# Kernel optimization log

Hardware: AMD Instinct MI355X
Metric: run time of the kernel (lower is better)

Reference implementation:

```python
import jax, jax.numpy as jnp
import numpy as np

H = 8          # n_heads
MRF = 128      # max_rf random features
EPS = 1e-4


def fiber2head(feats, h):
    # feats: list of [N, m_d, 2d+1] -> [N, h, sum_d (m_d/h)*(2d+1)]
    N = feats[0].shape[0]
    return jnp.concatenate([f.reshape(N, h, -1) for f in feats], axis=-1)


def softmax_kernel(data, w, is_query):
    # FAVOR+ positive random features. data: [B,H,L,d], w: [m,d]
    dn = data.shape[-1] ** -0.25
    ratio = w.shape[0] ** -0.5
    dd = jnp.einsum('bhld,md->bhlm', data * dn, w)
    diag = (data * data).sum(-1, keepdims=True) * (0.5 * dn * dn)
    if is_query:
        mx = jax.lax.stop_gradient(dd.max(-1, keepdims=True))
    else:
        mx = jax.lax.stop_gradient(dd.max())
    return ratio * (jnp.exp(dd - diag - mx) + EPS)


def setup_inputs() -> dict:
    key = jax.random.key(0)
    ks = jax.random.split(key, 7)
    B, L = 4, 8192
    N = B * L
    v0 = jax.random.normal(ks[0], (N, 64, 1), jnp.float32)
    v1 = jax.random.normal(ks[1], (N, 64, 3), jnp.float32)
    k0 = jax.random.normal(ks[2], (N, 64, 1), jnp.float32)
    k1 = jax.random.normal(ks[3], (N, 64, 3), jnp.float32)
    q0 = jax.random.normal(ks[4], (N, 64, 1), jnp.float32)
    q1 = jax.random.normal(ks[5], (N, 64, 3), jnp.float32)
    w = jax.random.normal(ks[6], (MRF, 32), jnp.float32)  # random-feature projection
    return {'v0': v0, 'v1': v1, 'k0': k0, 'k1': k1, 'q0': q0, 'q1': q1, 'w': w, 'batch_size': 4}


def reference(v0, v1, k0, k1, q0, q1, w, batch_size):
    B = batch_size
    N = v0.shape[0]
    L = N // B
    # Q from the k-dict (as in source); source then overwrites K with Q, so the
    # q-dict features are mathematically unused.
    Q = fiber2head([k0, k1], H).reshape(B, L, H, -1).transpose(0, 2, 1, 3)  # [B,H,L,d_k]
    K = Q  # faithful to `K = Q.view(...)` in the source
    Kp = softmax_kernel(K, w, is_query=False)  # [B,H,L,m]
    Qp = softmax_kernel(Q, w, is_query=True)   # [B,H,L,m]
    # Normalizer is identical for every value channel (q/k are expanded copies).
    D_inv = 1.0 / jnp.einsum('bhlm,bhm->bhl', Qp, Kp.sum(axis=2))
    outs = []
    for v in (v0, v1):
        m, e = v.shape[1], v.shape[2]     # multiplicity, 2d+1
        c = m // H                         # channels per head
        vv = v.reshape(B, L, H, c, e).transpose(0, 2, 3, 1, 4)  # [B,H,c,L,e]
        # linear attention: context [B,H,c,m,e] is small -> O(L*m*e) traffic
        ctx = jnp.einsum('bhlm,bhcle->bhcme', Kp, vv)
        o = jnp.einsum('bhcme,bhlm,bhl->bhcle', ctx, Qp, D_inv)
        o = o.reshape(B, H * c, L, e).transpose(0, 2, 1, 3).reshape(B * L, c * H, e)
        outs.append(o)
    return tuple(outs)  # (out_deg0 [N,64,1], out_deg1 [N,64,3])
```

## Files before the change

### kernel.cpp

```cpp
#include <hip/hip_runtime.h>

#define BB 4
#define HH 8
#define LL 8192
#define NN (BB*LL)
#define DDIM 32
#define MM 128

#define CTXR_OFF 0
#define KSUMR_OFF (CTXR_OFF + 32*8*MM*4)
#define VSUM_OFF  (KSUMR_OFF + 32*MM)
#define GMAX_OFF  (VSUM_OFF + 32*32)
#define ZERO_FLOATS (GMAX_OFF + 1)

#define DN 0.42044820762685725f
#define RATIO 0.08838834764831845f
#define EPSF 1e-4f

#define ACC_UPDATE(kp, a0, a1, b4)                                     \
    do {                                                               \
        acc[0]  = fmaf(kp,(a0).x,acc[0]);   acc[4]  = fmaf(kp,(a0).y,acc[4]);  \
        acc[8]  = fmaf(kp,(a0).z,acc[8]);   acc[12] = fmaf(kp,(a0).w,acc[12]); \
        acc[16] = fmaf(kp,(a1).x,acc[16]);  acc[20] = fmaf(kp,(a1).y,acc[20]); \
        acc[24] = fmaf(kp,(a1).z,acc[24]);  acc[28] = fmaf(kp,(a1).w,acc[28]); \
        float4 g;                                                      \
        g = (b4)[0];                                                   \
        acc[1]=fmaf(kp,g.x,acc[1]);  acc[2]=fmaf(kp,g.y,acc[2]);       \
        acc[3]=fmaf(kp,g.z,acc[3]);  acc[5]=fmaf(kp,g.w,acc[5]);       \
        g = (b4)[1];                                                   \
        acc[6]=fmaf(kp,g.x,acc[6]);  acc[7]=fmaf(kp,g.y,acc[7]);       \
        acc[9]=fmaf(kp,g.z,acc[9]);  acc[10]=fmaf(kp,g.w,acc[10]);     \
        g = (b4)[2];                                                   \
        acc[11]=fmaf(kp,g.x,acc[11]); acc[13]=fmaf(kp,g.y,acc[13]);    \
        acc[14]=fmaf(kp,g.z,acc[14]); acc[15]=fmaf(kp,g.w,acc[15]);    \
        g = (b4)[3];                                                   \
        acc[17]=fmaf(kp,g.x,acc[17]); acc[18]=fmaf(kp,g.y,acc[18]);    \
        acc[19]=fmaf(kp,g.z,acc[19]); acc[21]=fmaf(kp,g.w,acc[21]);    \
        g = (b4)[4];                                                   \
        acc[22]=fmaf(kp,g.x,acc[22]); acc[23]=fmaf(kp,g.y,acc[23]);    \
        acc[25]=fmaf(kp,g.z,acc[25]); acc[26]=fmaf(kp,g.w,acc[26]);    \
        g = (b4)[5];                                                   \
        acc[27]=fmaf(kp,g.x,acc[27]); acc[29]=fmaf(kp,g.y,acc[29]);    \
        acc[30]=fmaf(kp,g.z,acc[30]); acc[31]=fmaf(kp,g.w,acc[31]);    \
    } while (0)

__global__ __launch_bounds__(256, 2) void k_ctx1(const float* __restrict__ kk0,
                                                 const float* __restrict__ kk1,
                                                 const float* __restrict__ v0,
                                                 const float* __restrict__ v1,
                                                 const float* __restrict__ w,
                                                 float* __restrict__ ws) {
    __shared__ float red[2][64][34];
    const int tid = threadIdx.x;
    const int lane = tid & 63;
    const int wv  = __builtin_amdgcn_readfirstlane(tid >> 6);
    const int bh = blockIdx.x >> 6;
    const int chunk = (blockIdx.x >> 1) & 31;
    const int mhalf = blockIdx.x & 1;
    const int m = mhalf*64 + lane;
    const int b = bh >> 3, h = bh & 7;
    const int n0 = b*LL + chunk*256 + wv*64;
    float wreg[32];
    {
        const float4* w4 = (const float4*)(w + m*DDIM);
#pragma unroll
        for (int q = 0; q < 8; ++q) {
            const float4 t = w4[q];
            wreg[q*4+0]=t.x*DN; wreg[q*4+1]=t.y*DN;
            wreg[q*4+2]=t.z*DN; wreg[q*4+3]=t.w*DN;
        }
    }
    float acc[32];
#pragma unroll
    for (int i = 0; i < 32; ++i) acc[i] = 0.f;
    float ksum_acc = 0.f, vsum_acc = 0.f, wmax = -3.4e38f;
    for (int s = 0; s < 4; ++s) {
        const int nb = n0 + s*16;
        const int dr_ = lane >> 2, dq = lane & 3;
        float diagv;
        {
            const int n = nb + dr_;
            float4 da, db;
            if (dq == 0) {
                da = *(const float4*)(kk0 + (size_t)n*64 + h*8);
                db = *(const float4*)(kk0 + (size_t)n*64 + h*8 + 4);
            } else {
                const float* bp = kk1 + (size_t)n*192 + h*24 + (dq-1)*8;
                da = *(const float4*)bp; db = *(const float4*)(bp + 4);
            }
            float ss = da.x*da.x+da.y*da.y+da.z*da.z+da.w*da.w
                     + db.x*db.x+db.y*db.y+db.z*db.z+db.w*db.w;
            ss += __shfl_xor(ss, 1); ss += __shfl_xor(ss, 2);
            diagv = 0.5f*DN*DN*ss;
        }
        if (mhalf == 0) {
            const int ve = lane & 31, vg = lane >> 5;
#pragma unroll
            for (int rr = 0; rr < 8; ++rr) {
                const int n = nb + vg*8 + rr;
                vsum_acc += (ve < 8) ? v0[(size_t)n*64 + h*8 + ve]
                                     : v1[(size_t)n*192 + h*24 + (ve-8)];
            }
        }
#pragma unroll 1
        for (int r = 0; r < 16; r += 2) {
            const int nA = nb + r, nB = nb + r + 1;
            const float dgA = __uint_as_float(
                __builtin_amdgcn_readlane(__float_as_uint(diagv), r*4));
            const float dgB = __uint_as_float(
                __builtin_amdgcn_readlane(__float_as_uint(diagv), r*4 + 4));
            float4 kA[8], kB[8];
            kA[0] = *(const float4*)(kk0 + (size_t)nA*64 + h*8);
            kA[1] = *(const float4*)(kk0 + (size_t)nA*64 + h*8 + 4);
            kB[0] = *(const float4*)(kk0 + (size_t)nB*64 + h*8);
            kB[1] = *(const float4*)(kk0 + (size_t)nB*64 + h*8 + 4);
            {
                const float4* gA4 = (const float4*)(kk1 + (size_t)nA*192 + h*24);
                const float4* gB4 = (const float4*)(kk1 + (size_t)nB*192 + h*24);
#pragma unroll
                for (int gq = 0; gq < 6; ++gq) { kA[2+gq] = gA4[gq]; kB[2+gq] = gB4[gq]; }
            }
            float ddA0 = 0.f, ddA1 = 0.f, ddB0 = 0.f, ddB1 = 0.f;
#pragma unroll
            for (int q = 0; q < 8; ++q) {
                ddA0 = fmaf(kA[q].x, wreg[q*4+0], ddA0);
                ddB0 = fmaf(kB[q].x, wreg[q*4+0], ddB0);
                ddA1 = fmaf(kA[q].y, wreg[q*4+1], ddA1);
                ddB1 = fmaf(kB[q].y, wreg[q*4+1], ddB1);
                ddA0 = fmaf(kA[q].z, wreg[q*4+2], ddA0);
                ddB0 = fmaf(kB[q].z, wreg[q*4+2], ddB0);
                ddA1 = fmaf(kA[q].w, wreg[q*4+3], ddA1);
                ddB1 = fmaf(kB[q].w, wreg[q*4+3], ddB1);
            }
            const float ddA = ddA0 + ddA1;
            const float ddB = ddB0 + ddB1;
            wmax = fmaxf(wmax, fmaxf(ddA, ddB));
            const float kpA = __expf(ddA - dgA);
            const float kpB = __expf(ddB - dgB);
            ksum_acc += kpA; ksum_acc += kpB;
            const float4 aA0 = *(const float4*)(v0 + (size_t)nA*64 + h*8);
            const float4 aA1 = *(const float4*)(v0 + (size_t)nA*64 + h*8 + 4);
            const float4 aB0 = *(const float4*)(v0 + (size_t)nB*64 + h*8);
            const float4 aB1 = *(const float4*)(v0 + (size_t)nB*64 + h*8 + 4);
            const float4* bA4 = (const float4*)(v1 + (size_t)nA*192 + h*24);
            const float4* bB4 = (const float4*)(v1 + (size_t)nB*192 + h*24);
            ACC_UPDATE(kpA, aA0, aA1, bA4);
            ACC_UPDATE(kpB, aB0, aB1, bB4);
        }
    }
    if (wv == 1 || wv == 3) {
        float (*rp)[34] = red[wv >> 1];
#pragma unroll
        for (int i = 0; i < 32; ++i) rp[lane][i] = acc[i];
        rp[lane][32] = ksum_acc;
        rp[lane][33] = vsum_acc;
    }
    __syncthreads();
    if (wv == 0 || wv == 2) {
        float (*rp)[34] = red[wv >> 1];
#pragma unroll
        for (int i = 0; i < 32; ++i) acc[i] += rp[lane][i];
        ksum_acc += rp[lane][32];
        vsum_acc += rp[lane][33];
    }
    __syncthreads();
    if (wv == 2) {
#pragma unroll
        for (int i = 0; i < 32; ++i) red[0][lane][i] = acc[i];
        red[0][lane][32] = ksum_acc;
        red[0][lane][33] = vsum_acc;
    }
    __syncthreads();
    if (wv == 0) {
#pragma unroll
        for (int i = 0; i < 32; ++i) acc[i] += red[0][lane][i];
        ksum_acc += red[0][lane][32];
        vsum_acc += red[0][lane][33];
        float* ctxr = ws + CTXR_OFF;
#pragma unroll
        for (int c = 0; c < 8; ++c)
#pragma unroll
            for (int j = 0; j < 4; ++j)
                atomicAdd(&ctxr[((bh*8 + c)*MM + m)*4 + j], acc[c*4+j]);
        atomicAdd(ws + KSUMR_OFF + bh*MM + m, ksum_acc);
        if (mhalf == 0) {
            const int ve = lane & 31;
            const int packed = (ve < 8) ? ve*4
                                        : ((ve-8)/3)*4 + 1 + (ve-8)%3;
            atomicAdd(ws + VSUM_OFF + bh*32 + packed, vsum_acc);
        }
    }
#pragma unroll
    for (int off = 32; off; off >>= 1) wmax = fmaxf(wmax, __shfl_xor(wmax, off, 64));
    if (lane == 0) {
        unsigned u = __float_as_uint(wmax);
        u = (u & 0x80000000u) ? ~u : (u | 0x80000000u);
        atomicMax((unsigned*)(ws + GMAX_OFF), u);
    }
}

__global__ __launch_bounds__(256, 1) void k_out(const float* __restrict__ kk0,
                                                const float* __restrict__ kk1,
                                                const float* __restrict__ w,
                                                const float* __restrict__ ws,
                                                float* __restrict__ out) {
    __shared__ float ctx_s[128*36];
    __shared__ float wlds[128*36];
    __shared__ float ksl[128];
    __shared__ __align__(16) float sS0[32];
    __shared__ float sK0;
    const int tid = threadIdx.x;
    const int bh = blockIdx.x >> 4, chunk = blockIdx.x & 15;
    const int b = bh >> 3, h = bh & 7;
    const unsigned gu = *((const unsigned*)(ws + GMAX_OFF));
    const float gm = (gu & 0x80000000u) ? __uint_as_float(gu & 0x7fffffffu)
                                        : __uint_as_float(~gu);
    const float alpha = __expf(-gm);
    const float4* ctxr4 = (const float4*)(ws + CTXR_OFF) + (size_t)bh*1024;
    const float* vsg = ws + VSUM_OFF + bh*32;
#pragma unroll
    for (int it = 0; it < 4; ++it) {
        const int i = tid + it*256;
        const int c = i >> 7, mm2 = i & 127;
        const float4 q = ctxr4[i];
        const int p0 = c*4;
        ctx_s[mm2*36+p0+0] = RATIO*(alpha*q.x + EPSF*vsg[p0+0]);
        ctx_s[mm2*36+p0+1] = RATIO*(alpha*q.y + EPSF*vsg[p0+1]);
        ctx_s[mm2*36+p0+2] = RATIO*(alpha*q.z + EPSF*vsg[p0+2]);
        ctx_s[mm2*36+p0+3] = RATIO*(alpha*q.w + EPSF*vsg[p0+3]);
    }
    {
        const float4* w4 = (const float4*)w;
#pragma unroll
        for (int it = 0; it < 4; ++it) {
            const int i = tid + it*256;
            const int mm2 = i >> 3, q = i & 7;
            float4 t = w4[i];
            t.x*=DN; t.y*=DN; t.z*=DN; t.w*=DN;
            *(float4*)&wlds[mm2*36+q*4] = t;
        }
    }
    if (tid < 128) ksl[tid] = RATIO*(alpha*ws[KSUMR_OFF + bh*MM + tid] + EPSF*(float)LL);
    __syncthreads();
    if (tid < 32) {
        float s = 0.f;
#pragma unroll 8
        for (int mm2 = 0; mm2 < 128; ++mm2) s += ctx_s[mm2*36 + tid];
        sS0[tid] = s;
    } else if (tid < 64) {
        const int p2 = tid - 32;
        float s = ksl[p2] + ksl[32+p2] + ksl[64+p2] + ksl[96+p2];
        s += __shfl_xor(s, 1); s += __shfl_xor(s, 2); s += __shfl_xor(s, 4);
        s += __shfl_xor(s, 8); s += __shfl_xor(s, 16);
        if (p2 == 0) sK0 = s;
    }
    __syncthreads();
    const int nA = b*LL + chunk*512 + tid;
    const int nB = nA + 256;
    float KA[32], KB[32];
    {
        const float4 f0 = *(const float4*)(kk0 + (size_t)nA*64 + h*8);
        const float4 f1 = *(const float4*)(kk0 + (size_t)nA*64 + h*8 + 4);
        KA[0]=f0.x; KA[1]=f0.y; KA[2]=f0.z; KA[3]=f0.w;
        KA[4]=f1.x; KA[5]=f1.y; KA[6]=f1.z; KA[7]=f1.w;
        const float4 g0 = *(const float4*)(kk0 + (size_t)nB*64 + h*8);
        const float4 g1 = *(const float4*)(kk0 + (size_t)nB*64 + h*8 + 4);
        KB[0]=g0.x; KB[1]=g0.y; KB[2]=g0.z; KB[3]=g0.w;
        KB[4]=g1.x; KB[5]=g1.y; KB[6]=g1.z; KB[7]=g1.w;
        const float4* a4 = (const float4*)(kk1 + (size_t)nA*192 + h*24);
        const float4* b4 = (const float4*)(kk1 + (size_t)nB*192 + h*24);
#pragma unroll
        for (int gq = 0; gq < 6; ++gq) {
            const float4 ga = a4[gq];
            KA[8+gq*4+0]=ga.x; KA[8+gq*4+1]=ga.y; KA[8+gq*4+2]=ga.z; KA[8+gq*4+3]=ga.w;
            const float4 gb = b4[gq];
            KB[8+gq*4+0]=gb.x; KB[8+gq*4+1]=gb.y; KB[8+gq*4+2]=gb.z; KB[8+gq*4+3]=gb.w;
        }
    }
    float dgA = 0.f, dgB = 0.f;
#pragma unroll
    for (int d = 0; d < 32; ++d) { dgA = fmaf(KA[d], KA[d], dgA); dgB = fmaf(KB[d], KB[d], dgB); }
    dgA *= 0.5f*DN*DN;  dgB *= 0.5f*DN*DN;
    float S1A[32], S1B[32];
#pragma unroll
    for (int i = 0; i < 32; ++i) { S1A[i] = 0.f; S1B[i] = 0.f; }
    float denA = 0.f, denB = 0.f, mxA = -3.4e38f, mxB = -3.4e38f;
#pragma unroll 1
    for (int m2 = 0; m2 < 128; ++m2) {
        const float* wrow = &wlds[m2*36];
        float dA0 = 0.f, dA1 = 0.f, dB0 = 0.f, dB1 = 0.f;
#pragma unroll
        for (int q = 0; q < 8; ++q) {
            const float4 wv = *(const float4*)&wrow[q*4];
            dA0 = fmaf(KA[q*4+0], wv.x, dA0);
            dB0 = fmaf(KB[q*4+0], wv.x, dB0);
            dA1 = fmaf(KA[q*4+1], wv.y, dA1);
            dB1 = fmaf(KB[q*4+1], wv.y, dB1);
            dA0 = fmaf(KA[q*4+2], wv.z, dA0);
            dB0 = fmaf(KB[q*4+2], wv.z, dB0);
            dA1 = fmaf(KA[q*4+3], wv.w, dA1);
            dB1 = fmaf(KB[q*4+3], wv.w, dB1);
        }
        const float ddA = dA0 + dA1;
        const float ddB = dB0 + dB1;
        mxA = fmaxf(mxA, ddA);
        mxB = fmaxf(mxB, ddB);
        const float EA = __expf(ddA - dgA);
        const float EB = __expf(ddB - dgB);
        denA = fmaf(EA, ksl[m2], denA);
        denB = fmaf(EB, ksl[m2], denB);
        const float* crow = &ctx_s[m2*36];
#pragma unroll
        for (int q = 0; q < 8; ++q) {
            const float4 cv = *(const float4*)&crow[q*4];
            S1A[q*4+0] = fmaf(EA, cv.x, S1A[q*4+0]);
            S1B[q*4+0] = fmaf(EB, cv.x, S1B[q*4+0]);
            S1A[q*4+1] = fmaf(EA, cv.y, S1A[q*4+1]);
            S1B[q*4+1] = fmaf(EB, cv.y, S1B[q*4+1]);
            S1A[q*4+2] = fmaf(EA, cv.z, S1A[q*4+2]);
            S1B[q*4+2] = fmaf(EB, cv.z, S1B[q*4+2]);
            S1A[q*4+3] = fmaf(EA, cv.w, S1A[q*4+3]);
            S1B[q*4+3] = fmaf(EB, cv.w, S1B[q*4+3]);
        }
    }
    const float esA = __expf(-mxA);
    const float esB = __expf(-mxB);
    const float dinvA = 1.f / fmaf(esA, denA, EPSF*sK0);
    const float dinvB = 1.f / fmaf(esB, denB, EPSF*sK0);
    float vA[32], vB[32];
#pragma unroll
    for (int q = 0; q < 8; ++q) {
        const float4 s0 = *(const float4*)&sS0[q*4];
        vA[q*4+0] = fmaf(esA, S1A[q*4+0], EPSF*s0.x)*dinvA;
        vA[q*4+1] = fmaf(esA, S1A[q*4+1], EPSF*s0.y)*dinvA;
        vA[q*4+2] = fmaf(esA, S1A[q*4+2], EPSF*s0.z)*dinvA;
        vA[q*4+3] = fmaf(esA, S1A[q*4+3], EPSF*s0.w)*dinvA;
        vB[q*4+0] = fmaf(esB, S1B[q*4+0], EPSF*s0.x)*dinvB;
        vB[q*4+1] = fmaf(esB, S1B[q*4+1], EPSF*s0.y)*dinvB;
        vB[q*4+2] = fmaf(esB, S1B[q*4+2], EPSF*s0.z)*dinvB;
        vB[q*4+3] = fmaf(esB, S1B[q*4+3], EPSF*s0.w)*dinvB;
    }
    {
        float* o0 = out + (size_t)nA*64 + h*8;
        *(float4*)(o0)     = make_float4(vA[0],  vA[4],  vA[8],  vA[12]);
        *(float4*)(o0 + 4) = make_float4(vA[16], vA[20], vA[24], vA[28]);
        float* o1 = out + (size_t)NN*64 + (size_t)nA*192 + h*24;
        *(float4*)(o1 +  0) = make_float4(vA[1],  vA[2],  vA[3],  vA[5]);
        *(float4*)(o1 +  4) = make_float4(vA[6],  vA[7],  vA[9],  vA[10]);
        *(float4*)(o1 +  8) = make_float4(vA[11], vA[13], vA[14], vA[15]);
        *(float4*)(o1 + 12) = make_float4(vA[17], vA[18], vA[19], vA[21]);
        *(float4*)(o1 + 16) = make_float4(vA[22], vA[23], vA[25], vA[26]);
        *(float4*)(o1 + 20) = make_float4(vA[27], vA[29], vA[30], vA[31]);
    }
    {
        float* o0 = out + (size_t)nB*64 + h*8;
        *(float4*)(o0)     = make_float4(vB[0],  vB[4],  vB[8],  vB[12]);
        *(float4*)(o0 + 4) = make_float4(vB[16], vB[20], vB[24], vB[28]);
        float* o1 = out + (size_t)NN*64 + (size_t)nB*192 + h*24;
        *(float4*)(o1 +  0) = make_float4(vB[1],  vB[2],  vB[3],  vB[5]);
        *(float4*)(o1 +  4) = make_float4(vB[6],  vB[7],  vB[9],  vB[10]);
        *(float4*)(o1 +  8) = make_float4(vB[11], vB[13], vB[14], vB[15]);
        *(float4*)(o1 + 12) = make_float4(vB[17], vB[18], vB[19], vB[21]);
        *(float4*)(o1 + 16) = make_float4(vB[22], vB[23], vB[25], vB[26]);
        *(float4*)(o1 + 20) = make_float4(vB[27], vB[29], vB[30], vB[31]);
    }
}

extern "C" void kernel_launch(void* const* d_in, const int* in_sizes, int n_in,
                              void* d_out, int out_size, void* d_ws, size_t ws_size,
                              hipStream_t stream) {
    const float* v0 = (const float*)d_in[0];
    const float* v1 = (const float*)d_in[1];
    const float* k0 = (const float*)d_in[2];
    const float* k1 = (const float*)d_in[3];
    const float* w  = (const float*)d_in[6];
    float* out = (float*)d_out;
    float* ws  = (float*)d_ws;
    hipMemsetAsync(ws, 0, (size_t)ZERO_FLOATS*sizeof(float), stream);
    k_ctx1<<<2048, 256, 0, stream>>>(k0, k1, v0, v1, w, ws);
    k_out <<<512, 256, 0, stream>>>(k0, k1, w, ws, out);
}
```

Before: 259.9 us.

## Load K/V tiles cooperatively across lanes and broadcast via readlane

In the context-accumulation kernel, each lane no longer issues redundant wave-uniform loads of the same K and V rows. Lanes now cooperatively load a 32-row tile into registers with distributed float4 loads, and every scalar is broadcast with v_readlane in fully unrolled loops. This removes duplicated global/L1 load traffic and address arithmetic per row. In exchange it adds many readlane (SALU/VALU) instructions and larger unrolled code, with more register pressure.

Result: faster. 243.8 us (-6.2%).

```diff
diff --git a/kernel.cpp b/kernel.cpp
--- a/kernel.cpp
+++ b/kernel.cpp
@@ -17,32 +17,13 @@
 #define RATIO 0.08838834764831845f
 #define EPSF 1e-4f
 
-#define ACC_UPDATE(kp, a0, a1, b4)                                     \
-    do {                                                               \
-        acc[0]  = fmaf(kp,(a0).x,acc[0]);   acc[4]  = fmaf(kp,(a0).y,acc[4]);  \
-        acc[8]  = fmaf(kp,(a0).z,acc[8]);   acc[12] = fmaf(kp,(a0).w,acc[12]); \
-        acc[16] = fmaf(kp,(a1).x,acc[16]);  acc[20] = fmaf(kp,(a1).y,acc[20]); \
-        acc[24] = fmaf(kp,(a1).z,acc[24]);  acc[28] = fmaf(kp,(a1).w,acc[28]); \
-        float4 g;                                                      \
-        g = (b4)[0];                                                   \
-        acc[1]=fmaf(kp,g.x,acc[1]);  acc[2]=fmaf(kp,g.y,acc[2]);       \
-        acc[3]=fmaf(kp,g.z,acc[3]);  acc[5]=fmaf(kp,g.w,acc[5]);       \
-        g = (b4)[1];                                                   \
-        acc[6]=fmaf(kp,g.x,acc[6]);  acc[7]=fmaf(kp,g.y,acc[7]);       \
-        acc[9]=fmaf(kp,g.z,acc[9]);  acc[10]=fmaf(kp,g.w,acc[10]);     \
-        g = (b4)[2];                                                   \
-        acc[11]=fmaf(kp,g.x,acc[11]); acc[13]=fmaf(kp,g.y,acc[13]);    \
-        acc[14]=fmaf(kp,g.z,acc[14]); acc[15]=fmaf(kp,g.w,acc[15]);    \
-        g = (b4)[3];                                                   \
-        acc[17]=fmaf(kp,g.x,acc[17]); acc[18]=fmaf(kp,g.y,acc[18]);    \
-        acc[19]=fmaf(kp,g.z,acc[19]); acc[21]=fmaf(kp,g.w,acc[21]);    \
-        g = (b4)[4];                                                   \
-        acc[22]=fmaf(kp,g.x,acc[22]); acc[23]=fmaf(kp,g.y,acc[23]);    \
-        acc[25]=fmaf(kp,g.z,acc[25]); acc[26]=fmaf(kp,g.w,acc[26]);    \
-        g = (b4)[5];                                                   \
-        acc[27]=fmaf(kp,g.x,acc[27]); acc[29]=fmaf(kp,g.y,acc[29]);    \
-        acc[30]=fmaf(kp,g.z,acc[30]); acc[31]=fmaf(kp,g.w,acc[31]);    \
-    } while (0)
+__device__ __forceinline__ float rl(float x, int l) {
+    return __uint_as_float(__builtin_amdgcn_readlane(__float_as_uint(x), l));
+}
+__device__ __forceinline__ float rl4(float4 v, int c, int l) {
+    const float x = (c==0) ? v.x : (c==1) ? v.y : (c==2) ? v.z : v.w;
+    return rl(x, l);
+}
 
 __global__ __launch_bounds__(256, 2) void k_ctx1(const float* __restrict__ kk0,
                                                  const float* __restrict__ kk1,
@@ -70,16 +51,30 @@
             wreg[q*4+2]=t.z*DN; wreg[q*4+3]=t.w*DN;
         }
     }
+    const int rowA = lane >> 1, qA = lane & 1;
+    const int offA = rowA*64 + h*8 + qA*4;
+    const int rowB = lane >> 3, qB = lane & 7;
+    const int offB = rowB*192 + h*24 + ((qB < 6) ? qB*4 : 20);
     float acc[32];
 #pragma unroll
     for (int i = 0; i < 32; ++i) acc[i] = 0.f;
     float ksum_acc = 0.f, vsum_acc = 0.f, wmax = -3.4e38f;
-    for (int s = 0; s < 4; ++s) {
-        const int nb = n0 + s*16;
-        const int dr_ = lane >> 2, dq = lane & 3;
-        float diagv;
-        {
-            const int n = nb + dr_;
+#pragma unroll 1
+    for (int bi = 0; bi < 2; ++bi) {
+        const int nb = n0 + bi*32;
+        const float4 k0b = *(const float4*)(kk0 + (size_t)nb*64 + offA);
+        const float4 v0b = *(const float4*)(v0  + (size_t)nb*64 + offA);
+        float4 k1b[4], v1b[4];
+#pragma unroll
+        for (int j = 0; j < 4; ++j) {
+            k1b[j] = *(const float4*)(kk1 + (size_t)nb*192 + j*1536 + offB);
+            v1b[j] = *(const float4*)(v1  + (size_t)nb*192 + j*1536 + offB);
+        }
+        float diagv0, diagv1;
+#pragma unroll
+        for (int dp = 0; dp < 2; ++dp) {
+            const int dr_ = lane >> 2, dq = lane & 3;
+            const int n = nb + dp*16 + dr_;
             float4 da, db;
             if (dq == 0) {
                 da = *(const float4*)(kk0 + (size_t)n*64 + h*8);
@@ -91,61 +86,55 @@
             float ss = da.x*da.x+da.y*da.y+da.z*da.z+da.w*da.w
                      + db.x*db.x+db.y*db.y+db.z*db.z+db.w*db.w;
             ss += __shfl_xor(ss, 1); ss += __shfl_xor(ss, 2);
-            diagv = 0.5f*DN*DN*ss;
+            const float dv_ = 0.5f*DN*DN*ss;
+            if (dp == 0) diagv0 = dv_; else diagv1 = dv_;
         }
         if (mhalf == 0) {
             const int ve = lane & 31, vg = lane >> 5;
 #pragma unroll
+            for (int dp = 0; dp < 2; ++dp)
+#pragma unroll
+                for (int rr = 0; rr < 8; ++rr) {
+                    const int n = nb + dp*16 + vg*8 + rr;
+                    vsum_acc += (ve < 8) ? v0[(size_t)n*64 + h*8 + ve]
+                                         : v1[(size_t)n*192 + h*24 + (ve-8)];
+                }
+        }
+#pragma unroll
+        for (int rq = 0; rq < 4; ++rq) {
+#pragma unroll
             for (int rr = 0; rr < 8; ++rr) {
-                const int n = nb + vg*8 + rr;
-                vsum_acc += (ve < 8) ? v0[(size_t)n*64 + h*8 + ve]
-                                     : v1[(size_t)n*192 + h*24 + (ve-8)];
+                const int r = rq*8 + rr;
+                const float dg = rl((r < 16) ? diagv0 : diagv1, (r & 15)*4);
+                float dd0 = 0.f, dd1 = 0.f;
+#pragma unroll
+                for (int d = 0; d < 8; ++d) {
+                    const float s = rl4(k0b, d & 3, r*2 + (d >> 2));
+                    if (d & 1) dd1 = fmaf(s, wreg[d], dd1);
+                    else       dd0 = fmaf(s, wreg[d], dd0);
+                }
+#pragma unroll
+                for (int e = 0; e < 24; ++e) {
+                    const float s = rl4(k1b[rq], e & 3, rr*8 + (e >> 2));
+                    if (e & 1) dd1 = fmaf(s, wreg[8+e], dd1);
+                    else       dd0 = fmaf(s, wreg[8+e], dd0);
+                }
+                const float dd = dd0 + dd1;
+                wmax = fmaxf(wmax, dd);
+                const float kp = __expf(dd - dg);
+                ksum_acc += kp;
+#pragma unroll
+                for (int c = 0; c < 8; ++c) {
+                    const float av = rl4(v0b, c & 3, r*2 + (c >> 2));
+                    acc[c*4] = fmaf(kp, av, acc[c*4]);
+                }
+#pragma unroll
+                for (int e = 0; e < 24; ++e) {
+                    const float av = rl4(v1b[rq], e & 3, rr*8 + (e >> 2));
+                    const int ai = (e/3)*4 + 1 + e%3;
+                    acc[ai] = fmaf(kp, av, acc[ai]);
+                }
             }
-        }
-#pragma unroll 1
-        for (int r = 0; r < 16; r += 2) {
-            const int nA = nb + r, nB = nb + r + 1;
-            const float dgA = __uint_as_float(
-                __builtin_amdgcn_readlane(__float_as_uint(diagv), r*4));
-            const float dgB = __uint_as_float(
-                __builtin_amdgcn_readlane(__float_as_uint(diagv), r*4 + 4));
-            float4 kA[8], kB[8];
-            kA[0] = *(const float4*)(kk0 + (size_t)nA*64 + h*8);
-            kA[1] = *(const float4*)(kk0 + (size_t)nA*64 + h*8 + 4);
-            kB[0] = *(const float4*)(kk0 + (size_t)nB*64 + h*8);
-            kB[1] = *(const float4*)(kk0 + (size_t)nB*64 + h*8 + 4);
-            {
-                const float4* gA4 = (const float4*)(kk1 + (size_t)nA*192 + h*24);
-                const float4* gB4 = (const float4*)(kk1 + (size_t)nB*192 + h*24);
-#pragma unroll
-                for (int gq = 0; gq < 6; ++gq) { kA[2+gq] = gA4[gq]; kB[2+gq] = gB4[gq]; }
-            }
-            float ddA0 = 0.f, ddA1 = 0.f, ddB0 = 0.f, ddB1 = 0.f;
-#pragma unroll
-            for (int q = 0; q < 8; ++q) {
-                ddA0 = fmaf(kA[q].x, wreg[q*4+0], ddA0);
-                ddB0 = fmaf(kB[q].x, wreg[q*4+0], ddB0);
-                ddA1 = fmaf(kA[q].y, wreg[q*4+1], ddA1);
-                ddB1 = fmaf(kB[q].y, wreg[q*4+1], ddB1);
-                ddA0 = fmaf(kA[q].z, wreg[q*4+2], ddA0);
-                ddB0 = fmaf(kB[q].z, wreg[q*4+2], ddB0);
-                ddA1 = fmaf(kA[q].w, wreg[q*4+3], ddA1);
-                ddB1 = fmaf(kB[q].w, wreg[q*4+3], ddB1);
-            }
-            const float ddA = ddA0 + ddA1;
-            const float ddB = ddB0 + ddB1;
-            wmax = fmaxf(wmax, fmaxf(ddA, ddB));
-            const float kpA = __expf(ddA - dgA);
-            const float kpB = __expf(ddB - dgB);
-            ksum_acc += kpA; ksum_acc += kpB;
-            const float4 aA0 = *(const float4*)(v0 + (size_t)nA*64 + h*8);
-            const float4 aA1 = *(const float4*)(v0 + (size_t)nA*64 + h*8 + 4);
-            const float4 aB0 = *(const float4*)(v0 + (size_t)nB*64 + h*8);
-            const float4 aB1 = *(const float4*)(v0 + (size_t)nB*64 + h*8 + 4);
-            const float4* bA4 = (const float4*)(v1 + (size_t)nA*192 + h*24);
-            const float4* bB4 = (const float4*)(v1 + (size_t)nB*192 + h*24);
-            ACC_UPDATE(kpA, aA0, aA1, bA4);
-            ACC_UPDATE(kpB, aB0, aB1, bB4);
         }
     }
     if (wv == 1 || wv == 3) {
```
